# Kernel tuning notes

Hardware: AMD Instinct MI355X
Metric: run time of the kernel (lower is better)

The kernel has to match this reference:

```python
import jax, jax.numpy as jnp
import numpy as np

B, N, D, R, K = 4096, 50, 128, 3, 128  # batch, triples/pair, embed dim, n_relations, r_dim


def setup_inputs() -> dict:
    key = jax.random.key(0)
    ks = jax.random.split(key, 8)
    scale_w = (2.0 / (2 * D + K)) ** 0.5  # xavier_normal for [2D, K]
    scale_r = (2.0 / (R + K)) ** 0.5
    return {
        "u_emb": jax.random.normal(ks[0], (B, D), jnp.float32),
        "i_emb": jax.random.normal(ks[1], (B, D), jnp.float32),
        "a_emb": jax.random.normal(ks[2], (B, N, D), jnp.float32),
        "o_emb": jax.random.normal(ks[3], (B, N, D), jnp.float32),
        "w_aor": jax.random.normal(ks[4], (R, 2 * D, K), jnp.float32) * scale_w,
        "w_uir": jax.random.normal(ks[5], (R, 2 * D, K), jnp.float32) * scale_w,
        "r_param": jax.random.normal(ks[6], (R, K), jnp.float32) * scale_r,
        "s": jax.random.randint(ks[7], (B, N), 0, R, jnp.int32),
    }


def reference(u_emb, i_emb, a_emb, o_emb, w_aor, w_uir, r_param, s):
    # transr branch of AOSPredictionLayer with loss='bpr'.
    ui_in = jnp.concatenate([u_emb, i_emb], axis=-1)      # [B, 2D]
    ao_in = jnp.concatenate([a_emb, o_emb], axis=-1)      # [B, N, 2D]
    # Compute per-relation projections for all R (R is tiny), then gather by s.
    # Equivalent to the masked gather->matmul->scatter loop in the original.
    ui_all = jnp.einsum('bd,rdk->brk', ui_in, w_uir) + r_param[None]   # [B, R, K]
    ao_all = jnp.einsum('bnd,rdk->bnrk', ao_in, w_aor)                 # [B, N, R, K]
    s = s.astype(jnp.int32)
    ui_emb = jnp.take_along_axis(ui_all, s[..., None], axis=1)         # [B, N, K]
    ao_emb = jnp.take_along_axis(ao_all, s[..., None, None], axis=2)[..., 0, :]  # [B, N, K]
    # bpr loss head: dot product score
    return jnp.sum(ui_emb * ao_emb, axis=-1)              # [B, N]
```

## Files before the change

kernel.cpp:

```cpp
#include <hip/hip_runtime.h>


#define TWO_D 256
#define RD 768

__global__ __launch_bounds__(256) void relproj_kernel(
    const float* __restrict__ w_aor, const float* __restrict__ w_uir,
    const float* __restrict__ r_param, float* __restrict__ w2t,
    float* __restrict__ cvec)
{
    const int r  = blockIdx.z;
    const int d0 = blockIdx.x * 64;
    const int p0 = blockIdx.y * 64;
    const int tid = threadIdx.x;
    const int tx = tid & 15, ty = tid >> 4;

    __shared__ float4 a4[64][16];
    __shared__ float4 b4[64][16];

    float acc[4][4];
#pragma unroll
    for (int i = 0; i < 4; ++i)
#pragma unroll
        for (int j = 0; j < 4; ++j) acc[i][j] = 0.f;

    const float* Am = w_aor + (size_t)r * 256 * 128;
    const float* Bm = w_uir + (size_t)r * 256 * 128;

    for (int ks = 0; ks < 2; ++ks) {
        const int kb = ks * 64;
        __syncthreads();
#pragma unroll
        for (int i = 0; i < 4; ++i) {
            int f = tid + i * 256;
            int row = f >> 4, k4 = f & 15;
            int slot = k4 ^ ((row >> 2) & 15);
            a4[row][slot] = *(const float4*)(Am + (size_t)(d0 + row) * 128 + kb + k4 * 4);
            b4[row][slot] = *(const float4*)(Bm + (size_t)(p0 + row) * 128 + kb + k4 * 4);
        }
        __syncthreads();
#pragma unroll
        for (int k4 = 0; k4 < 16; ++k4) {
            float4 av[4], bv[4];
#pragma unroll
            for (int i = 0; i < 4; ++i) { int m = ty * 4 + i; av[i] = a4[m][k4 ^ ((m >> 2) & 15)]; }
#pragma unroll
            for (int j = 0; j < 4; ++j) { int n = tx * 4 + j; bv[j] = b4[n][k4 ^ ((n >> 2) & 15)]; }
#pragma unroll
            for (int i = 0; i < 4; ++i)
#pragma unroll
                for (int j = 0; j < 4; ++j)
                    acc[i][j] += av[i].x * bv[j].x + av[i].y * bv[j].y +
                                 av[i].z * bv[j].z + av[i].w * bv[j].w;
        }
    }

#pragma unroll
    for (int i = 0; i < 4; ++i) {
        int m = ty * 4 + i;
        float4 o = make_float4(acc[i][0], acc[i][1], acc[i][2], acc[i][3]);
        *(float4*)(w2t + (size_t)(r * 256 + d0 + m) * 256 + p0 + tx * 4) = o;
    }

    if (blockIdx.y == 0 && tid < 64) {
        int d = d0 + tid;
        const float* ar = Am + (size_t)d * 128;
        const float* rp = r_param + r * 128;
        float ssum = 0.f;
#pragma unroll 4
        for (int kk = 0; kk < 128; ++kk) ssum += ar[kk] * rp[kk];
        cvec[r * 256 + d] = ssum;
    }
}

__global__ __launch_bounds__(256) void vproj_kernel(
    const float* __restrict__ u_emb, const float* __restrict__ i_emb,
    const float* __restrict__ w2t, const float* __restrict__ cvec,
    float* __restrict__ v)
{
    const int b0 = blockIdx.x * 64;
    const int n0 = blockIdx.y * 32;
    const int tid = threadIdx.x;
    const int tx = tid & 15, ty = tid >> 4;

    __shared__ float4 a4[64][16];
    __shared__ float4 b4[32][16];

    float acc[4][2];
#pragma unroll
    for (int i = 0; i < 4; ++i) { acc[i][0] = 0.f; acc[i][1] = 0.f; }

    for (int ks = 0; ks < 4; ++ks) {
        const float* srcA = ((ks < 2) ? u_emb : i_emb) + (ks & 1) * 64;
        const float* srcB = w2t + ks * 64;
        __syncthreads();
#pragma unroll
        for (int i = 0; i < 4; ++i) {
            int f = tid + i * 256;
            int row = f >> 4, k4 = f & 15;
            a4[row][k4 ^ ((row >> 2) & 15)] =
                *(const float4*)(srcA + (size_t)(b0 + row) * 128 + k4 * 4);
        }
#pragma unroll
        for (int i = 0; i < 2; ++i) {
            int f = tid + i * 256;
            int row = f >> 4, k4 = f & 15;
            b4[row][k4 ^ ((row >> 2) & 15)] =
                *(const float4*)(srcB + (size_t)(n0 + row) * 256 + k4 * 4);
        }
        __syncthreads();
#pragma unroll
        for (int k4 = 0; k4 < 16; ++k4) {
            float4 av[4], bv[2];
#pragma unroll
            for (int i = 0; i < 4; ++i) { int m = ty * 4 + i; av[i] = a4[m][k4 ^ ((m >> 2) & 15)]; }
#pragma unroll
            for (int j = 0; j < 2; ++j) { int n = tx * 2 + j; bv[j] = b4[n][k4 ^ ((n >> 2) & 15)]; }
#pragma unroll
            for (int i = 0; i < 4; ++i)
#pragma unroll
                for (int j = 0; j < 2; ++j)
                    acc[i][j] += av[i].x * bv[j].x + av[i].y * bv[j].y +
                                 av[i].z * bv[j].z + av[i].w * bv[j].w;
        }
    }

    const float2 cb = *(const float2*)(cvec + n0 + tx * 2);
#pragma unroll
    for (int i = 0; i < 4; ++i) {
        int m = ty * 4 + i;
        float2 o = make_float2(acc[i][0] + cb.x, acc[i][1] + cb.y);
        *(float2*)(v + (size_t)(b0 + m) * RD + n0 + tx * 2) = o;
    }
}

__global__ __launch_bounds__(256) void score_kernel(
    const float* __restrict__ a_emb, const float* __restrict__ o_emb,
    const float* __restrict__ v, const int* __restrict__ s,
    float* __restrict__ out)
{
    const int b = blockIdx.x;
    const int tid = threadIdx.x;
    const int w = tid >> 6, l = tid & 63;
    const int ll = l & 31, half = l >> 5;
    const size_t rowbase = (size_t)b * 50;

    const float4* a4p = (const float4*)a_emb;
    const float4* o4p = (const float4*)o_emb;

    float4 xa[6], xo[6];
#pragma unroll
    for (int p = 0; p < 6; ++p) {
        const int n = p * 8 + w * 2 + half;
        const size_t base4 = (rowbase + n) * 32 + ll;
        xa[p] = a4p[base4];
        xo[p] = o4p[base4];
    }
    float4 xa6 = make_float4(0.f, 0.f, 0.f, 0.f);
    float4 xo6 = xa6;
    if (w == 0) {
        const size_t base4 = (rowbase + 48 + half) * 32 + ll;
        xa6 = a4p[base4];
        xo6 = o4p[base4];
    }

    __shared__ float4 v4[192];
    __shared__ int sl[52];
    if (tid < 192) v4[tid] = ((const float4*)(v + (size_t)b * RD))[tid];
    if (tid < 50) sl[tid] = s[rowbase + tid];
    __syncthreads();

#pragma unroll
    for (int p = 0; p < 6; ++p) {
        const int n = p * 8 + w * 2 + half;
        const int rel = sl[n];
        const float4 va = v4[rel * 64 + ll];
        const float4 vo = v4[rel * 64 + 32 + ll];
        float ps = xa[p].x * va.x + xa[p].y * va.y + xa[p].z * va.z + xa[p].w * va.w
                 + xo[p].x * vo.x + xo[p].y * vo.y + xo[p].z * vo.z + xo[p].w * vo.w;
#pragma unroll
        for (int off = 16; off >= 1; off >>= 1) ps += __shfl_xor(ps, off, 64);
        if (ll == 0) out[rowbase + n] = ps;
    }
    if (w == 0) {
        const int n = 48 + half;
        const int rel = sl[n];
        const float4 va = v4[rel * 64 + ll];
        const float4 vo = v4[rel * 64 + 32 + ll];
        float ps = xa6.x * va.x + xa6.y * va.y + xa6.z * va.z + xa6.w * va.w
                 + xo6.x * vo.x + xo6.y * vo.y + xo6.z * vo.z + xo6.w * vo.w;
#pragma unroll
        for (int off = 16; off >= 1; off >>= 1) ps += __shfl_xor(ps, off, 64);
        if (ll == 0) out[rowbase + n] = ps;
    }
}

extern "C" void kernel_launch(void* const* d_in, const int* in_sizes, int n_in,
                              void* d_out, int out_size, void* d_ws, size_t ws_size,
                              hipStream_t stream)
{
    const float* u_emb   = (const float*)d_in[0];
    const float* i_emb   = (const float*)d_in[1];
    const float* a_emb   = (const float*)d_in[2];
    const float* o_emb   = (const float*)d_in[3];
    const float* w_aor   = (const float*)d_in[4];
    const float* w_uir   = (const float*)d_in[5];
    const float* r_param = (const float*)d_in[6];
    const int*   s       = (const int*)d_in[7];
    float* out = (float*)d_out;

    float* v    = (float*)d_ws;
    float* w2t  = v + (size_t)4096 * RD;
    float* cvec = w2t + (size_t)RD * TWO_D;

    relproj_kernel<<<dim3(4, 4, 3), 256, 0, stream>>>(w_aor, w_uir, r_param, w2t, cvec);
    vproj_kernel<<<dim3(4096 / 64, RD / 32), 256, 0, stream>>>(u_emb, i_emb, w2t, cvec, v);
    score_kernel<<<4096, 256, 0, stream>>>(a_emb, o_emb, v, s, out);
}
```

Measured before the change: 293.2 us.

## Stream score-kernel inputs via global_load_lds and process eight batches per block

The score kernel now copies a_emb, o_emb and v rows straight into LDS with the AMD global_load_lds builtin instead of loading them into registers. Each block loops over eight batch rows, with 512 blocks instead of 4096. The intent is to cut register pressure and launch overhead on this memory-bound stream. In exchange, the loop is serialized with two barriers per iteration and nothing is double-buffered, so loads are not overlapped with compute within a block.

```diff
diff --git a/kernel.cpp b/kernel.cpp
--- a/kernel.cpp
+++ b/kernel.cpp
@@ -3,6 +3,13 @@
 
 #define TWO_D 256
 #define RD 768
+
+typedef __attribute__((address_space(1))) const unsigned int g_u32;
+typedef __attribute__((address_space(3))) unsigned int l_u32;
+
+static __device__ __forceinline__ void gl_lds16(const void* g, void* l) {
+    __builtin_amdgcn_global_load_lds((g_u32*)g, (l_u32*)l, 16, 0, 0);
+}
 
 __global__ __launch_bounds__(256) void relproj_kernel(
     const float* __restrict__ w_aor, const float* __restrict__ w_uir,
@@ -139,59 +146,49 @@
     const float* __restrict__ v, const int* __restrict__ s,
     float* __restrict__ out)
 {
-    const int b = blockIdx.x;
+    __shared__ float aL[4][1792];
+    __shared__ float oL[4][1792];
+    __shared__ float vL[768];
+    __shared__ int   sL[64];
+
     const int tid = threadIdx.x;
     const int w = tid >> 6, l = tid & 63;
     const int ll = l & 31, half = l >> 5;
-    const size_t rowbase = (size_t)b * 50;
-
-    const float4* a4p = (const float4*)a_emb;
-    const float4* o4p = (const float4*)o_emb;
-
-    float4 xa[6], xo[6];
-#pragma unroll
-    for (int p = 0; p < 6; ++p) {
-        const int n = p * 8 + w * 2 + half;
-        const size_t base4 = (rowbase + n) * 32 + ll;
-        xa[p] = a4p[base4];
-        xo[p] = o4p[base4];
-    }
-    float4 xa6 = make_float4(0.f, 0.f, 0.f, 0.f);
-    float4 xo6 = xa6;
-    if (w == 0) {
-        const size_t base4 = (rowbase + 48 + half) * 32 + ll;
-        xa6 = a4p[base4];
-        xo6 = o4p[base4];
-    }
-
-    __shared__ float4 v4[192];
-    __shared__ int sl[52];
-    if (tid < 192) v4[tid] = ((const float4*)(v + (size_t)b * RD))[tid];
-    if (tid < 50) sl[tid] = s[rowbase + tid];
-    __syncthreads();
-
-#pragma unroll
-    for (int p = 0; p < 6; ++p) {
-        const int n = p * 8 + w * 2 + half;
-        const int rel = sl[n];
-        const float4 va = v4[rel * 64 + ll];
-        const float4 vo = v4[rel * 64 + 32 + ll];
-        float ps = xa[p].x * va.x + xa[p].y * va.y + xa[p].z * va.z + xa[p].w * va.w
-                 + xo[p].x * vo.x + xo[p].y * vo.y + xo[p].z * vo.z + xo[p].w * vo.w;
-#pragma unroll
-        for (int off = 16; off >= 1; off >>= 1) ps += __shfl_xor(ps, off, 64);
-        if (ll == 0) out[rowbase + n] = ps;
-    }
-    if (w == 0) {
-        const int n = 48 + half;
-        const int rel = sl[n];
-        const float4 va = v4[rel * 64 + ll];
-        const float4 vo = v4[rel * 64 + 32 + ll];
-        float ps = xa6.x * va.x + xa6.y * va.y + xa6.z * va.z + xa6.w * va.w
-                 + xo6.x * vo.x + xo6.y * vo.y + xo6.z * vo.z + xo6.w * vo.w;
-#pragma unroll
-        for (int off = 16; off >= 1; off >>= 1) ps += __shfl_xor(ps, off, 64);
-        if (ll == 0) out[rowbase + n] = ps;
+    const int rs = w * 14;
+    const int npair = (w < 3) ? 7 : 4;
+
+    for (int i = 0; i < 8; ++i) {
+        const int b = blockIdx.x * 8 + i;
+        const size_t rowbase = (size_t)b * 50;
+
+        for (int j = 0; j < npair; ++j) {
+            gl_lds16(a_emb + (rowbase + rs + 2 * j) * 128 + l * 4, &aL[w][j * 256]);
+            gl_lds16(o_emb + (rowbase + rs + 2 * j) * 128 + l * 4, &oL[w][j * 256]);
+        }
+        if (w == 0) {
+#pragma unroll
+            for (int j = 0; j < 3; ++j)
+                gl_lds16(v + (size_t)b * RD + j * 256 + l * 4, &vL[j * 256]);
+        }
+        if (tid < 50) sL[tid] = s[rowbase + tid];
+        __syncthreads();
+
+#pragma unroll 2
+        for (int r = 0; r < npair; ++r) {
+            const int lr = 2 * r + half;
+            const int n  = rs + lr;
+            const int rel = sL[n];
+            const float4 xa = *(const float4*)(&aL[w][lr * 128 + ll * 4]);
+            const float4 xo = *(const float4*)(&oL[w][lr * 128 + ll * 4]);
+            const float4 va = *(const float4*)(&vL[rel * 256 + ll * 4]);
+            const float4 vo = *(const float4*)(&vL[rel * 256 + 128 + ll * 4]);
+            float ps = xa.x * va.x + xa.y * va.y + xa.z * va.z + xa.w * va.w
+                     + xo.x * vo.x + xo.y * vo.y + xo.z * vo.z + xo.w * vo.w;
+#pragma unroll
+            for (int off = 16; off >= 1; off >>= 1) ps += __shfl_xor(ps, off, 64);
+            if (ll == 0) out[rowbase + n] = ps;
+        }
+        __syncthreads();
     }
 }
 
@@ -215,5 +212,5 @@
 
     relproj_kernel<<<dim3(4, 4, 3), 256, 0, stream>>>(w_aor, w_uir, r_param, w2t, cvec);
     vproj_kernel<<<dim3(4096 / 64, RD / 32), 256, 0, stream>>>(u_emb, i_emb, w2t, cvec, v);
-    score_kernel<<<4096, 256, 0, stream>>>(a_emb, o_emb, v, s, out);
-}
+    score_kernel<<<512, 256, 0, stream>>>(a_emb, o_emb, v, s, out);
+}
```

Result: no change. 297.9 us (+1.6%).
